# Kernel optimization log

Measured on AMD Instinct MI355X. Metric: run time of the kernel, lower is better.

The kernel has to match this reference:

```python
import jax, jax.numpy as jnp
import numpy as np

TOP_K = 2


def setup_inputs() -> dict:
    key = jax.random.key(0)
    k0, k1, k2, k3, k4 = jax.random.split(key, 5)
    B, S, D, E, F = 4, 2048, 1024, 8, 512
    return {
        "hidden_states": jax.random.normal(k0, (B, S, D), dtype=jnp.float32),
        "router_weight": jax.random.normal(k1, (E, D), dtype=jnp.float32) * 0.02,
        "w_gate": jax.random.normal(k2, (E, D, F), dtype=jnp.float32) * 0.02,
        "w_up": jax.random.normal(k3, (E, D, F), dtype=jnp.float32) * 0.02,
        "w_down": jax.random.normal(k4, (E, F, D), dtype=jnp.float32) * 0.02,
    }


def reference(hidden_states, router_weight, w_gate, w_up, w_down):
    B, S, D = hidden_states.shape
    E = router_weight.shape[0]
    x = hidden_states.reshape(-1, D)          # [T, D] token-flattened
    T = x.shape[0]

    # --- TopKRouter: softmax over experts, top-k, renormalize selected probs ---
    logits = x @ router_weight.T              # [T, E]
    probs = jax.nn.softmax(logits, axis=-1)
    top_p, top_i = jax.lax.top_k(probs, TOP_K)            # [T, k]
    top_p = top_p / jnp.sum(top_p, axis=-1, keepdims=True)  # renormalize=True

    # combine weights: scatter selected probabilities into [T, E]
    combine = jnp.zeros((T, E), x.dtype).at[jnp.arange(T)[:, None], top_i].add(top_p)

    # --- Grouped SwiGLU experts (dropless: zero combine weight => zero contribution) ---
    g = jnp.einsum('td,edf->tef', x, w_gate)  # [T, E, F]
    u = jnp.einsum('td,edf->tef', x, w_up)    # [T, E, F]
    h = jax.nn.silu(g) * u                    # SwiGLU activation
    # down-proj + weighted combine fused
    out = jnp.einsum('tef,efd,te->td', h, w_down, combine)  # [T, D]
    return out.reshape(B, S, D)
```

## Files before the change

kernel.cpp:

```cpp
#include <hip/hip_runtime.h>
#include <hip/hip_bf16.h>


typedef __attribute__((ext_vector_type(4))) float  f32x4;
typedef __attribute__((ext_vector_type(8))) unsigned short us8;
typedef __attribute__((ext_vector_type(4))) unsigned short us4;
typedef __bf16 bf16_t;
typedef __attribute__((ext_vector_type(8))) bf16_t bf16x8;

#define TTOK 8192
#define DDIM 1024
#define EEXP 8
#define FDIM 512

__device__ __forceinline__ unsigned short f2bf(float f) {
  unsigned int u = __float_as_uint(f);
  u = (u + 0x7FFFu + ((u >> 16) & 1u)) >> 16;
  return (unsigned short)u;
}

__device__ __forceinline__ void gload16(const void* g, void* l) {
  __builtin_amdgcn_global_load_lds(
      (const __attribute__((address_space(1))) void*)g,
      (__attribute__((address_space(3))) void*)l, 16, 0, 0);
}

__global__ __launch_bounds__(256) void k_cvt_x(const float* __restrict__ x,
                                               unsigned short* __restrict__ xb) {
  int i = blockIdx.x * 256 + threadIdx.x;
  const f32x4* s = (const f32x4*)x + (size_t)i * 2;
  f32x4 a = s[0], b = s[1];
  us8 o;
  o[0]=f2bf(a[0]); o[1]=f2bf(a[1]); o[2]=f2bf(a[2]); o[3]=f2bf(a[3]);
  o[4]=f2bf(b[0]); o[5]=f2bf(b[1]); o[6]=f2bf(b[2]); o[7]=f2bf(b[3]);
  *((us8*)xb + i) = o;
}

__global__ __launch_bounds__(256) void k_tcvt(const float* __restrict__ src,
                                              unsigned short* __restrict__ dst,
                                              int M, int N) {
  __shared__ float tile[32][33];
  int e  = blockIdx.z;
  int m0 = blockIdx.y * 32, n0 = blockIdx.x * 32;
  const float* s = src + (size_t)e * M * N;
  unsigned short* d = dst + (size_t)e * M * N;
  int r  = threadIdx.x >> 3;
  int c4 = (threadIdx.x & 7) * 4;
  f32x4 v = *(const f32x4*)(s + (size_t)(m0 + r) * N + n0 + c4);
  tile[r][c4+0] = v[0]; tile[r][c4+1] = v[1];
  tile[r][c4+2] = v[2]; tile[r][c4+3] = v[3];
  __syncthreads();
  us4 o;
  o[0] = f2bf(tile[c4+0][r]); o[1] = f2bf(tile[c4+1][r]);
  o[2] = f2bf(tile[c4+2][r]); o[3] = f2bf(tile[c4+3][r]);
  *(us4*)(d + (size_t)(n0 + r) * M + m0 + c4) = o;
}

__global__ __launch_bounds__(256) void k_router(const float* __restrict__ x,
                                                const float* __restrict__ rw,
                                                int* __restrict__ topki,
                                                float* __restrict__ topkw) {
  __shared__ float wlds[8 * 1024];
  int tid = threadIdx.x;
  #pragma unroll
  for (int i = 0; i < 8; ++i)
    ((f32x4*)wlds)[tid + i * 256] = ((const f32x4*)rw)[tid + i * 256];
  __syncthreads();

  int wv = tid >> 6, lane = tid & 63;
  int t = blockIdx.x * 4 + wv;
  const f32x4* xr = (const f32x4*)(x + (size_t)t * DDIM);
  f32x4 xv[4];
  #pragma unroll
  for (int j = 0; j < 4; ++j) xv[j] = xr[j * 64 + lane];
  double xd[16];
  #pragma unroll
  for (int j = 0; j < 4; ++j) {
    xd[j*4+0] = xv[j][0]; xd[j*4+1] = xv[j][1];
    xd[j*4+2] = xv[j][2]; xd[j*4+3] = xv[j][3];
  }
  float pf[8];
  #pragma unroll
  for (int e = 0; e < 8; ++e) {
    double acc = 0.0;
    #pragma unroll
    for (int j = 0; j < 4; ++j) {
      f32x4 wv4 = ((const f32x4*)(wlds + e * 1024))[j * 64 + lane];
      acc = fma((double)wv4[0], xd[j*4+0], acc);
      acc = fma((double)wv4[1], xd[j*4+1], acc);
      acc = fma((double)wv4[2], xd[j*4+2], acc);
      acc = fma((double)wv4[3], xd[j*4+3], acc);
    }
    pf[e] = (float)acc;
  }
  #pragma unroll
  for (int e = 0; e < 8; ++e) {
    #pragma unroll
    for (int off = 32; off >= 1; off >>= 1)
      pf[e] += __shfl_xor(pf[e], off, 64);
  }
  if (lane == 0) {
    int i1 = 0;
    #pragma unroll
    for (int e2 = 1; e2 < 8; ++e2) if (pf[e2] > pf[i1]) i1 = e2;
    int i2 = (i1 == 0) ? 1 : 0;
    #pragma unroll
    for (int e2 = 0; e2 < 8; ++e2) if (e2 != i1 && pf[e2] > pf[i2]) i2 = e2;
    float d21 = pf[i2] - pf[i1];
    float e1  = __expf(d21);
    float s   = 1.f + e1;
    topki[2*t]   = i1;       topki[2*t+1] = i2;
    topkw[2*t]   = 1.f / s;  topkw[2*t+1] = e1 / s;
  }
}

__global__ __launch_bounds__(256) void k_count(const int* __restrict__ topki,
                                               int* __restrict__ ctrs) {
  __shared__ int h[8];
  if (threadIdx.x < 8) h[threadIdx.x] = 0;
  __syncthreads();
  int i = blockIdx.x * 256 + threadIdx.x;
  atomicAdd(&h[topki[i]], 1);
  __syncthreads();
  if (threadIdx.x < 8) atomicAdd(&ctrs[threadIdx.x], h[threadIdx.x]);
}

__global__ void k_scan(int* __restrict__ ctrs) {
  if (threadIdx.x == 0 && blockIdx.x == 0) {
    ctrs[8] = 0;
    #pragma unroll
    for (int e = 0; e < 8; ++e) ctrs[9 + e] = ctrs[8 + e] + ctrs[e];
    #pragma unroll
    for (int e = 0; e < 8; ++e) ctrs[17 + e] = 0;
  }
}

__global__ __launch_bounds__(256) void k_scatter(const int* __restrict__ topki,
                                                 const float* __restrict__ topkw,
                                                 int* __restrict__ ctrs,
                                                 int* __restrict__ at,
                                                 float* __restrict__ aw) {
  __shared__ int lc[8], base[8];
  int tid = threadIdx.x;
  if (tid < 8) lc[tid] = 0;
  __syncthreads();
  int t = blockIdx.x * 256 + tid;
  int e0 = topki[2*t], e1 = topki[2*t+1];
  int r0 = atomicAdd(&lc[e0], 1);
  int r1 = atomicAdd(&lc[e1], 1);
  __syncthreads();
  if (tid < 8) base[tid] = atomicAdd(&ctrs[17 + tid], lc[tid]);
  __syncthreads();
  int a0 = ctrs[8 + e0] + base[e0] + r0;
  int a1 = ctrs[8 + e1] + base[e1] + r1;
  at[a0] = t; aw[a0] = topkw[2*t];
  at[a1] = t; aw[a1] = topkw[2*t+1];
}

__global__ __launch_bounds__(512, 2) void k_gateup(
    const unsigned short* __restrict__ xb,
    const unsigned short* __restrict__ wgt,
    const unsigned short* __restrict__ wut,
    const int* __restrict__ at,
    const int* __restrict__ ctrs,
    unsigned short* __restrict__ h) {
  int e    = blockIdx.z;
  int seg0 = ctrs[8 + e];
  int cnt  = ctrs[9 + e] - seg0;
  int row0 = blockIdx.y * 256;
  if (row0 >= cnt) return;
  int f0 = blockIdx.x * 128;

  __shared__ unsigned short lA [2][256 * 64];
  __shared__ unsigned short lBg[2][128 * 64];
  __shared__ unsigned short lBu[2][128 * 64];
  __shared__ int s_tok[256];

  int tid = threadIdx.x;
  if (tid < 256) {
    int rg = row0 + tid;
    s_tok[tid] = at[seg0 + ((rg < cnt) ? rg : 0)];
  }
  __syncthreads();

  const unsigned short* aSrc[4];
  size_t bOff[2];
  #pragma unroll
  for (int i = 0; i < 4; ++i) {
    int row = i * 64 + (tid >> 3);
    int su  = (tid & 7) ^ (row & 7);
    aSrc[i] = xb + (size_t)s_tok[row] * DDIM + su * 8;
  }
  #pragma unroll
  for (int j = 0; j < 2; ++j) {
    int row = j * 64 + (tid >> 3);
    int su  = (tid & 7) ^ (row & 7);
    bOff[j] = (size_t)row * DDIM + su * 8;
  }
  const unsigned short* bgBase = wgt + ((size_t)e * FDIM + f0) * DDIM;
  const unsigned short* buBase = wut + ((size_t)e * FDIM + f0) * DDIM;

  int w = tid >> 6, lane = tid & 63;
  int wr = (w >> 1) * 64, wc = (w & 1) * 64;

  f32x4 zero = {0.f, 0.f, 0.f, 0.f};
  f32x4 accg[4][4], accu[4][4];
  #pragma unroll
  for (int mt = 0; mt < 4; ++mt)
    #pragma unroll
    for (int nt = 0; nt < 4; ++nt) { accg[mt][nt] = zero; accu[mt][nt] = zero; }

  #pragma unroll
  for (int i = 0; i < 4; ++i) gload16(aSrc[i], &lA[0][(i * 512 + tid) * 8]);
  #pragma unroll
  for (int j = 0; j < 2; ++j) {
    gload16(bgBase + bOff[j], &lBg[0][(j * 512 + tid) * 8]);
    gload16(buBase + bOff[j], &lBu[0][(j * 512 + tid) * 8]);
  }
  __syncthreads();

  int cur = 0;
  for (int ks = 0; ks < DDIM / 64; ++ks) {
    if (ks + 1 < DDIM / 64) {
      int k1 = (ks + 1) * 64;
      int nx = cur ^ 1;
      #pragma unroll
      for (int i = 0; i < 4; ++i) gload16(aSrc[i] + k1, &lA[nx][(i * 512 + tid) * 8]);
      #pragma unroll
      for (int j = 0; j < 2; ++j) {
        gload16(bgBase + bOff[j] + k1, &lBg[nx][(j * 512 + tid) * 8]);
        gload16(buBase + bOff[j] + k1, &lBu[nx][(j * 512 + tid) * 8]);
      }
    }
    #pragma unroll
    for (int kk = 0; kk < 2; ++kk) {
      bf16x8 af[4];
      #pragma unroll
      for (int mt = 0; mt < 4; ++mt) {
        int ar = wr + mt * 16 + (lane & 15);
        int au = (kk * 4 + (lane >> 4)) ^ (ar & 7);
        af[mt] = *(const bf16x8*)&lA[cur][(ar * 8 + au) * 8];
      }
      #pragma unroll
      for (int nt = 0; nt < 4; ++nt) {
        int br = wc + nt * 16 + (lane & 15);
        int bu = (kk * 4 + (lane >> 4)) ^ (br & 7);
        bf16x8 bg = *(const bf16x8*)&lBg[cur][(br * 8 + bu) * 8];
        bf16x8 bv = *(const bf16x8*)&lBu[cur][(br * 8 + bu) * 8];
        #pragma unroll
        for (int mt = 0; mt < 4; ++mt) {
          accg[mt][nt] = __builtin_amdgcn_mfma_f32_16x16x32_bf16(af[mt], bg, accg[mt][nt], 0, 0, 0);
          accu[mt][nt] = __builtin_amdgcn_mfma_f32_16x16x32_bf16(af[mt], bv, accu[mt][nt], 0, 0, 0);
        }
      }
    }
    __syncthreads();
    cur ^= 1;
  }
  #pragma unroll
  for (int mt = 0; mt < 4; ++mt) {
    #pragma unroll
    for (int nt = 0; nt < 4; ++nt) {
      #pragma unroll
      for (int j = 0; j < 4; ++j) {
        int rl = wr + mt * 16 + (lane >> 4) * 4 + j;
        if (row0 + rl < cnt) {
          float g = accg[mt][nt][j], u = accu[mt][nt][j];
          float hv = g * (1.f / (1.f + __expf(-g))) * u;
          h[(size_t)(seg0 + row0 + rl) * FDIM + f0 + wc + nt * 16 + (lane & 15)] = f2bf(hv);
        }
      }
    }
  }
}

__global__ __launch_bounds__(512, 2) void k_down(
    const unsigned short* __restrict__ h,
    const unsigned short* __restrict__ wdt,
    const int* __restrict__ at,
    const float* __restrict__ aw,
    const int* __restrict__ ctrs,
    float* __restrict__ out) {
  int e    = blockIdx.z;
  int seg0 = ctrs[8 + e];
  int cnt  = ctrs[9 + e] - seg0;
  int row0 = blockIdx.y * 256;
  if (row0 >= cnt) return;
  int d0 = blockIdx.x * 256;

  __shared__ unsigned short lA[2][256 * 64];
  __shared__ unsigned short lB[2][256 * 64];
  __shared__ int   s_tok[256];
  __shared__ float s_w[256];

  int tid = threadIdx.x;
  if (tid < 256) {
    int rg = row0 + tid;
    int a  = seg0 + ((rg < cnt) ? rg : 0);
    s_tok[tid] = at[a];
    s_w[tid]   = aw[a];
  }
  __syncthreads();

  const unsigned short* aSrc[4];
  size_t bOff[4];
  #pragma unroll
  for (int i = 0; i < 4; ++i) {
    int row = i * 64 + (tid >> 3);
    int su  = (tid & 7) ^ (row & 7);
    int rr  = (row0 + row < cnt) ? row0 + row : 0;
    aSrc[i] = h + (size_t)(seg0 + rr) * FDIM + su * 8;
    bOff[i] = (size_t)row * FDIM + su * 8;
  }
  const unsigned short* bBase = wdt + ((size_t)e * DDIM + d0) * FDIM;

  int w = tid >> 6, lane = tid & 63;
  int wr = (w >> 1) * 64, wc = (w & 1) * 128;

  f32x4 zero = {0.f, 0.f, 0.f, 0.f};
  f32x4 acc[4][8];
  #pragma unroll
  for (int mt = 0; mt < 4; ++mt)
    #pragma unroll
    for (int nt = 0; nt < 8; ++nt) acc[mt][nt] = zero;

  #pragma unroll
  for (int i = 0; i < 4; ++i) {
    gload16(aSrc[i],         &lA[0][(i * 512 + tid) * 8]);
    gload16(bBase + bOff[i], &lB[0][(i * 512 + tid) * 8]);
  }
  __syncthreads();

  int cur = 0;
  for (int ks = 0; ks < FDIM / 64; ++ks) {
    if (ks + 1 < FDIM / 64) {
      int k1 = (ks + 1) * 64;
      int nx = cur ^ 1;
      #pragma unroll
      for (int i = 0; i < 4; ++i) {
        gload16(aSrc[i] + k1,         &lA[nx][(i * 512 + tid) * 8]);
        gload16(bBase + bOff[i] + k1, &lB[nx][(i * 512 + tid) * 8]);
      }
    }
    #pragma unroll
    for (int kk = 0; kk < 2; ++kk) {
      bf16x8 af[4];
      #pragma unroll
      for (int mt = 0; mt < 4; ++mt) {
        int ar = wr + mt * 16 + (lane & 15);
        int au = (kk * 4 + (lane >> 4)) ^ (ar & 7);
        af[mt] = *(const bf16x8*)&lA[cur][(ar * 8 + au) * 8];
      }
      #pragma unroll
      for (int nt = 0; nt < 8; ++nt) {
        int br = wc + nt * 16 + (lane & 15);
        int bu = (kk * 4 + (lane >> 4)) ^ (br & 7);
        bf16x8 bf = *(const bf16x8*)&lB[cur][(br * 8 + bu) * 8];
        #pragma unroll
        for (int mt = 0; mt < 4; ++mt)
          acc[mt][nt] = __builtin_amdgcn_mfma_f32_16x16x32_bf16(af[mt], bf, acc[mt][nt], 0, 0, 0);
      }
    }
    __syncthreads();
    cur ^= 1;
  }
  #pragma unroll
  for (int mt = 0; mt < 4; ++mt) {
    #pragma unroll
    for (int nt = 0; nt < 8; ++nt) {
      #pragma unroll
      for (int j = 0; j < 4; ++j) {
        int rl = wr + mt * 16 + (lane >> 4) * 4 + j;
        if (row0 + rl < cnt) {
          float v = acc[mt][nt][j] * s_w[rl];
          atomicAdd(out + (size_t)s_tok[rl] * DDIM + d0 + wc + nt * 16 + (lane & 15), v);
        }
      }
    }
  }
}

extern "C" void kernel_launch(void* const* d_in, const int* in_sizes, int n_in,
                              void* d_out, int out_size, void* d_ws, size_t ws_size,
                              hipStream_t stream) {
  (void)in_sizes; (void)n_in; (void)ws_size;
  const float* x  = (const float*)d_in[0];
  const float* rw = (const float*)d_in[1];
  const float* wg = (const float*)d_in[2];
  const float* wu = (const float*)d_in[3];
  const float* wd = (const float*)d_in[4];
  float* out = (float*)d_out;

  char* ws = (char*)d_ws;
  unsigned short* xb  = (unsigned short*)(ws + 0);
  unsigned short* wgt = (unsigned short*)(ws + 16777216);
  unsigned short* wut = (unsigned short*)(ws + 25165824);
  unsigned short* wdt = (unsigned short*)(ws + 33554432);
  unsigned short* hbuf= (unsigned short*)(ws + 41943040);
  float* topkw = (float*)(ws + 58720256);
  int*   topki = (int*)  (ws + 58785792);
  int*   at    = (int*)  (ws + 58851328);
  float* aw    = (float*)(ws + 58916864);
  int*   ctrs  = (int*)  (ws + 58982400);

  hipMemsetAsync(ctrs, 0, 256, stream);
  hipMemsetAsync(out, 0, (size_t)out_size * sizeof(float), stream);

  k_cvt_x<<<4096, 256, 0, stream>>>(x, xb);
  k_tcvt <<<dim3(16, 32, 8), 256, 0, stream>>>(wg, wgt, 1024, 512);
  k_tcvt <<<dim3(16, 32, 8), 256, 0, stream>>>(wu, wut, 1024, 512);
  k_tcvt <<<dim3(32, 16, 8), 256, 0, stream>>>(wd, wdt, 512, 1024);
  k_router<<<2048, 256, 0, stream>>>(x, rw, topki, topkw);
  k_count <<<64, 256, 0, stream>>>(topki, ctrs);
  k_scan  <<<1, 64, 0, stream>>>(ctrs);
  k_scatter<<<32, 256, 0, stream>>>(topki, topkw, ctrs, at, aw);
  k_gateup<<<dim3(4, 64, 8), 512, 0, stream>>>(xb, wgt, wut, at, ctrs, hbuf);
  k_down  <<<dim3(4, 64, 8), 512, 0, stream>>>(hbuf, wdt, at, aw, ctrs, out);
}
```

Baseline: 306.2 us.

## Fuse x bf16 conversion into router; replace atomic scatter-add with per-slot bf16 output and combine kernel

The bf16 conversion of the activations moves into the router kernel, which removes a separate pass over x. The down-projection no longer does fp32 atomicAdds into the output. It writes weighted per-slot results in bf16 to a buffer that reuses the xb workspace, and a new combine kernel gathers each token's two slots through a position table and sums them. This also drops the output memset. In exchange it adds a 16MB bf16 intermediate write and read, and rounds each expert contribution to bf16 before summing.

```diff
diff --git a/kernel.cpp b/kernel.cpp
--- a/kernel.cpp
+++ b/kernel.cpp
@@ -19,21 +19,14 @@
   return (unsigned short)u;
 }
 
+__device__ __forceinline__ float bf2f(unsigned short u) {
+  return __uint_as_float((unsigned int)u << 16);
+}
+
 __device__ __forceinline__ void gload16(const void* g, void* l) {
   __builtin_amdgcn_global_load_lds(
       (const __attribute__((address_space(1))) void*)g,
       (__attribute__((address_space(3))) void*)l, 16, 0, 0);
-}
-
-__global__ __launch_bounds__(256) void k_cvt_x(const float* __restrict__ x,
-                                               unsigned short* __restrict__ xb) {
-  int i = blockIdx.x * 256 + threadIdx.x;
-  const f32x4* s = (const f32x4*)x + (size_t)i * 2;
-  f32x4 a = s[0], b = s[1];
-  us8 o;
-  o[0]=f2bf(a[0]); o[1]=f2bf(a[1]); o[2]=f2bf(a[2]); o[3]=f2bf(a[3]);
-  o[4]=f2bf(b[0]); o[5]=f2bf(b[1]); o[6]=f2bf(b[2]); o[7]=f2bf(b[3]);
-  *((us8*)xb + i) = o;
 }
 
 __global__ __launch_bounds__(256) void k_tcvt(const float* __restrict__ src,
@@ -58,6 +51,7 @@
 
 __global__ __launch_bounds__(256) void k_router(const float* __restrict__ x,
                                                 const float* __restrict__ rw,
+                                                unsigned short* __restrict__ xb,
                                                 int* __restrict__ topki,
                                                 float* __restrict__ topkw) {
   __shared__ float wlds[8 * 1024];
@@ -73,6 +67,13 @@
   f32x4 xv[4];
   #pragma unroll
   for (int j = 0; j < 4; ++j) xv[j] = xr[j * 64 + lane];
+  #pragma unroll
+  for (int j = 0; j < 4; ++j) {
+    us4 o;
+    o[0] = f2bf(xv[j][0]); o[1] = f2bf(xv[j][1]);
+    o[2] = f2bf(xv[j][2]); o[3] = f2bf(xv[j][3]);
+    *(us4*)(xb + (size_t)t * DDIM + (j * 64 + lane) * 4) = o;
+  }
   double xd[16];
   #pragma unroll
   for (int j = 0; j < 4; ++j) {
@@ -139,7 +140,8 @@
                                                  const float* __restrict__ topkw,
                                                  int* __restrict__ ctrs,
                                                  int* __restrict__ at,
-                                                 float* __restrict__ aw) {
+                                                 float* __restrict__ aw,
+                                                 int* __restrict__ pos) {
   __shared__ int lc[8], base[8];
   int tid = threadIdx.x;
   if (tid < 8) lc[tid] = 0;
@@ -155,6 +157,7 @@
   int a1 = ctrs[8 + e1] + base[e1] + r1;
   at[a0] = t; aw[a0] = topkw[2*t];
   at[a1] = t; aw[a1] = topkw[2*t+1];
+  pos[2*t] = a0; pos[2*t+1] = a1;
 }
 
 __global__ __launch_bounds__(512, 2) void k_gateup(
@@ -277,10 +280,9 @@
 __global__ __launch_bounds__(512, 2) void k_down(
     const unsigned short* __restrict__ h,
     const unsigned short* __restrict__ wdt,
-    const int* __restrict__ at,
     const float* __restrict__ aw,
     const int* __restrict__ ctrs,
-    float* __restrict__ out) {
+    unsigned short* __restrict__ y2) {
   int e    = blockIdx.z;
   int seg0 = ctrs[8 + e];
   int cnt  = ctrs[9 + e] - seg0;
@@ -290,15 +292,12 @@
 
   __shared__ unsigned short lA[2][256 * 64];
   __shared__ unsigned short lB[2][256 * 64];
-  __shared__ int   s_tok[256];
   __shared__ float s_w[256];
 
   int tid = threadIdx.x;
   if (tid < 256) {
     int rg = row0 + tid;
-    int a  = seg0 + ((rg < cnt) ? rg : 0);
-    s_tok[tid] = at[a];
-    s_w[tid]   = aw[a];
+    s_w[tid] = aw[seg0 + ((rg < cnt) ? rg : 0)];
   }
   __syncthreads();
 
@@ -373,17 +372,35 @@
         int rl = wr + mt * 16 + (lane >> 4) * 4 + j;
         if (row0 + rl < cnt) {
           float v = acc[mt][nt][j] * s_w[rl];
-          atomicAdd(out + (size_t)s_tok[rl] * DDIM + d0 + wc + nt * 16 + (lane & 15), v);
+          y2[(size_t)(seg0 + row0 + rl) * DDIM + d0 + wc + nt * 16 + (lane & 15)] = f2bf(v);
         }
       }
     }
   }
+}
+
+__global__ __launch_bounds__(256) void k_combine(const unsigned short* __restrict__ y2,
+                                                 const int* __restrict__ pos,
+                                                 float* __restrict__ out) {
+  int idx = blockIdx.x * 256 + threadIdx.x;
+  int t = idx >> 7;
+  int c = idx & 127;
+  int a0 = pos[2*t], a1 = pos[2*t+1];
+  us8 v0 = *((const us8*)(y2 + (size_t)a0 * DDIM) + c);
+  us8 v1 = *((const us8*)(y2 + (size_t)a1 * DDIM) + c);
+  f32x4 o0, o1;
+  #pragma unroll
+  for (int m = 0; m < 4; ++m) o0[m] = bf2f(v0[m]) + bf2f(v1[m]);
+  #pragma unroll
+  for (int m = 0; m < 4; ++m) o1[m] = bf2f(v0[4+m]) + bf2f(v1[4+m]);
+  f32x4* dst = (f32x4*)(out + (size_t)t * DDIM + c * 8);
+  dst[0] = o0; dst[1] = o1;
 }
 
 extern "C" void kernel_launch(void* const* d_in, const int* in_sizes, int n_in,
                               void* d_out, int out_size, void* d_ws, size_t ws_size,
                               hipStream_t stream) {
-  (void)in_sizes; (void)n_in; (void)ws_size;
+  (void)in_sizes; (void)n_in; (void)ws_size; (void)out_size;
   const float* x  = (const float*)d_in[0];
   const float* rw = (const float*)d_in[1];
   const float* wg = (const float*)d_in[2];
@@ -395,6 +412,7 @@
   unsigned short* xb  = (unsigned short*)(ws + 0);
   unsigned short* wgt = (unsigned short*)(ws + 16777216);
   unsigned short* wut = (unsigned short*)(ws + 25165824);
+  unsigned short* y2  = (unsigned short*)(ws + 0);
   unsigned short* wdt = (unsigned short*)(ws + 33554432);
   unsigned short* hbuf= (unsigned short*)(ws + 41943040);
   float* topkw = (float*)(ws + 58720256);
@@ -402,18 +420,18 @@
   int*   at    = (int*)  (ws + 58851328);
   float* aw    = (float*)(ws + 58916864);
   int*   ctrs  = (int*)  (ws + 58982400);
+  int*   pos   = (int*)  (ws + 58982656);
 
   hipMemsetAsync(ctrs, 0, 256, stream);
-  hipMemsetAsync(out, 0, (size_t)out_size * sizeof(float), stream);
-
-  k_cvt_x<<<4096, 256, 0, stream>>>(x, xb);
+
+  k_router<<<2048, 256, 0, stream>>>(x, rw, xb, topki, topkw);
   k_tcvt <<<dim3(16, 32, 8), 256, 0, stream>>>(wg, wgt, 1024, 512);
   k_tcvt <<<dim3(16, 32, 8), 256, 0, stream>>>(wu, wut, 1024, 512);
   k_tcvt <<<dim3(32, 16, 8), 256, 0, stream>>>(wd, wdt, 512, 1024);
-  k_router<<<2048, 256, 0, stream>>>(x, rw, topki, topkw);
   k_count <<<64, 256, 0, stream>>>(topki, ctrs);
   k_scan  <<<1, 64, 0, stream>>>(ctrs);
-  k_scatter<<<32, 256, 0, stream>>>(topki, topkw, ctrs, at, aw);
+  k_scatter<<<32, 256, 0, stream>>>(topki, topkw, ctrs, at, aw, pos);
   k_gateup<<<dim3(4, 64, 8), 512, 0, stream>>>(xb, wgt, wut, at, ctrs, hbuf);
-  k_down  <<<dim3(4, 64, 8), 512, 0, stream>>>(hbuf, wdt, at, aw, ctrs, out);
-}
+  k_down  <<<dim3(4, 64, 8), 512, 0, stream>>>(hbuf, wdt, aw, ctrs, y2);
+  k_combine<<<4096, 256, 0, stream>>>(y2, pos, out);
+}
```

Result: faster. 272.3 us (-11.1%).
